# Kernel optimization log

Measured on AMD Instinct MI355X. Metric: run time of the kernel, lower is better.

Reference implementation:

```python
import jax, jax.numpy as jnp
import numpy as np

E, K = 8, 2            # num_experts, top_k
H, DFF = 1024, 2048    # embd_dim, d_ff
B, S = 4, 1024


def setup_inputs() -> dict:
    key = jax.random.key(0)
    ks = jax.random.split(key, 5)
    s_in = 1.0 / np.sqrt(H)
    s_ff = 1.0 / np.sqrt(DFF)
    return {
        "x": jax.random.normal(ks[0], (B, S, H), jnp.float32),
        "centroids": jax.random.normal(ks[1], (E, H), jnp.float32),
        # nn.Linear weights are [out, in]
        "gate_w": jax.random.normal(ks[2], (E, DFF, H), jnp.float32) * s_in,
        "up_w": jax.random.normal(ks[3], (E, DFF, H), jnp.float32) * s_in,
        "down_w": jax.random.normal(ks[4], (E, H, DFF), jnp.float32) * s_ff,
        "routing_bias": jnp.zeros((E,), jnp.float32),
    }


def reference(x, centroids, gate_w, up_w, down_w, routing_bias):
    Bb, Ss, Hh = x.shape
    xf = x.reshape(-1, Hh)  # [T, H]
    # sigmoid affinity router + (non-trainable) routing bias
    affinity = jax.nn.sigmoid(xf @ centroids.T)          # [T, E]
    topk_scores, topk_idx = jax.lax.top_k(affinity + routing_bias, K)  # [T, K]
    topk_w = jax.nn.softmax(topk_scores, axis=-1)        # [T, K]

    # Dense per-expert SwiGLU FFN on all tokens (same math as the
    # sort/gather grouped loop; selection happens in the gather below).
    g = jnp.einsum('th,efh->etf', xf, gate_w)            # [E, T, DFF]
    u = jnp.einsum('th,efh->etf', xf, up_w)              # [E, T, DFF]
    y = jnp.einsum('etf,ehf->eth', jax.nn.silu(g) * u, down_w)  # [E, T, H]

    yt = jnp.transpose(y, (1, 0, 2))                     # [T, E, H]
    sel = jnp.take_along_axis(yt, topk_idx[:, :, None], axis=1)  # [T, K, H]
    out_flat = jnp.sum(sel * topk_w[:, :, None], axis=1)  # [T, H]

    counts = jnp.bincount(topk_idx.ravel(), length=E)    # per-expert token counts
    return out_flat.reshape(Bb, Ss, Hh), counts
```

## Files before the change

### kernel.cpp

```cpp
#include <hip/hip_runtime.h>
#include <math.h>

constexpr int E = 8, H = 1024, DFF = 2048, T = 4096;
constexpr int TR = 8192;
constexpr int BK = 32;

typedef __bf16 bf16x8 __attribute__((ext_vector_type(8)));
typedef __bf16 bf16x4 __attribute__((ext_vector_type(4)));
typedef float f32x4 __attribute__((ext_vector_type(4)));

__device__ __forceinline__ void gload16(const void* g, void* l) {
    __builtin_amdgcn_global_load_lds(
        (const __attribute__((address_space(1))) unsigned int*)g,
        (__attribute__((address_space(3))) unsigned int*)l, 16, 0, 0);
}

__global__ __launch_bounds__(256) void k1_affinity(
    const float* __restrict__ x, const float* __restrict__ cent,
    const float* __restrict__ bias,
    int* __restrict__ se, float* __restrict__ sw) {
    __shared__ float cs[E * H];
    int tid = threadIdx.x;
    for (int i = tid; i < E * H / 4; i += 256)
        ((float4*)cs)[i] = ((const float4*)cent)[i];
    __syncthreads();

    int wave = tid >> 6, lane = tid & 63;
    int t = blockIdx.x * 4 + wave;
    const float4* xr = (const float4*)(x + (size_t)t * H);
    float acc[E] = {};
    #pragma unroll
    for (int it = 0; it < 4; it++) {
        float4 xv = xr[lane + it * 64];
        #pragma unroll
        for (int e = 0; e < E; e++) {
            float4 cv = ((const float4*)(cs + e * H))[lane + it * 64];
            acc[e] = fmaf(xv.x, cv.x, acc[e]);
            acc[e] = fmaf(xv.y, cv.y, acc[e]);
            acc[e] = fmaf(xv.z, cv.z, acc[e]);
            acc[e] = fmaf(xv.w, cv.w, acc[e]);
        }
    }
    #pragma unroll
    for (int off = 32; off; off >>= 1)
        #pragma unroll
        for (int e = 0; e < E; e++) acc[e] += __shfl_down(acc[e], off);

    if (lane == 0) {
        float s[E];
        #pragma unroll
        for (int e = 0; e < E; e++)
            s[e] = 1.0f / (1.0f + expf(-acc[e])) + bias[e];
        int i0 = 0;
        for (int e = 1; e < E; e++) if (s[e] > s[i0]) i0 = e;
        int i1 = -1;
        for (int e = 0; e < E; e++) {
            if (e == i0) continue;
            if (i1 < 0 || s[e] > s[i1]) i1 = e;
        }
        float m = fmaxf(s[i0], s[i1]);
        float w0 = expf(s[i0] - m), w1 = expf(s[i1] - m);
        float inv = 1.0f / (w0 + w1);
        se[2 * t] = i0;     sw[2 * t] = w0 * inv;
        se[2 * t + 1] = i1; sw[2 * t + 1] = w1 * inv;
    }
}

__global__ __launch_bounds__(256) void k1b_partition(
    const int* __restrict__ se, int* __restrict__ token_list,
    int* __restrict__ sp, int* __restrict__ cnt) {
    int e = blockIdx.x;
    int tid = threadIdx.x;
    int wave = tid >> 6, lane = tid & 63;
    __shared__ int wsum[4];
    int running = 0;
    for (int c0 = 0; c0 < 2 * T; c0 += 256) {
        int i = c0 + tid;
        bool pred = (se[i] == e);
        unsigned long long mask = __ballot(pred);
        int pos_in_wave = __popcll(mask & ((1ull << lane) - 1ull));
        if (lane == 0) wsum[wave] = __popcll(mask);
        __syncthreads();
        int wbase = 0;
        for (int w2 = 0; w2 < wave; w2++) wbase += wsum[w2];
        int total = wsum[0] + wsum[1] + wsum[2] + wsum[3];
        if (pred) {
            int p = running + wbase + pos_in_wave;
            token_list[e * T + p] = i >> 1;
            sp[i] = p;
        }
        running += total;
        __syncthreads();
    }
    if (tid == 0) cnt[e] = running;
}

__global__ void k15_offsets(const int* __restrict__ cnt, int* __restrict__ off,
                            float* __restrict__ out_counts) {
    if (threadIdx.x == 0) {
        int acc = 0;
        for (int e = 0; e < E; e++) { off[e] = acc; acc += cnt[e]; }
    }
    if (threadIdx.x < E) out_counts[threadIdx.x] = (float)cnt[threadIdx.x];
}

__global__ __launch_bounds__(256) void k_conv(const float* __restrict__ in,
                                              __bf16* __restrict__ out, int n4) {
    int i = blockIdx.x * 256 + threadIdx.x;
    if (i < n4) {
        float4 v = ((const float4*)in)[i];
        bf16x4 o = {(__bf16)v.x, (__bf16)v.y, (__bf16)v.z, (__bf16)v.w};
        ((bf16x4*)out)[i] = o;
    }
}

__global__ __launch_bounds__(256) void k2_gateup(
    const __bf16* __restrict__ xb, const __bf16* __restrict__ gwb,
    const __bf16* __restrict__ uwb, const int* __restrict__ cnt,
    const int* __restrict__ off, const int* __restrict__ token_list,
    __bf16* __restrict__ h) {
    int bid = blockIdx.x;
    int e = bid >> 10;
    int rem = bid & 1023;
    int mt = rem >> 5;
    int nt = rem & 31;
    int Me = cnt[e];
    if (mt * 128 >= Me) return;
    int offe = off[e];

    __shared__ __bf16 As[128 * 32];
    __shared__ __bf16 Bg[64 * 32];
    __shared__ __bf16 Bu[64 * 32];

    int tid = threadIdx.x;
    int lane = tid & 63, w = tid >> 6;
    int wm = w >> 1, wn = w & 1;

    int l0 = tid, l1 = 256 + tid;
    int ar0 = l0 >> 2, akq0 = (l0 & 3) ^ ((ar0 >> 1) & 3);
    int ar1 = l1 >> 2, akq1 = (l1 & 3) ^ ((ar1 >> 1) & 3);
    int row0 = mt * 128 + ar0; if (row0 >= Me) row0 = Me - 1;
    int row1 = mt * 128 + ar1; if (row1 >= Me) row1 = Me - 1;
    int tok0 = token_list[e * T + row0];
    int tok1 = token_list[e * T + row1];
    const __bf16* asrc0 = xb + (size_t)tok0 * H + akq0 * 8;
    const __bf16* asrc1 = xb + (size_t)tok1 * H + akq1 * 8;
    const __bf16* gsrc = gwb + ((size_t)e * DFF + nt * 64 + ar0) * H + akq0 * 8;
    const __bf16* usrc = uwb + ((size_t)e * DFF + nt * 64 + ar0) * H + akq0 * 8;

    f32x4 accg[4][2] = {};
    f32x4 accu[4][2] = {};

    int kq = lane >> 4;
    int m15 = lane & 15;

    for (int k0 = 0; k0 < H; k0 += BK) {
        gload16(asrc0 + k0, &As[l0 * 8]);
        gload16(asrc1 + k0, &As[l1 * 8]);
        gload16(gsrc + k0, &Bg[tid * 8]);
        gload16(usrc + k0, &Bu[tid * 8]);
        __syncthreads();

        bf16x8 af[4], gf[2], uf[2];
        #pragma unroll
        for (int i = 0; i < 4; i++) {
            int row = wm * 64 + i * 16 + m15;
            int slot = kq ^ ((row >> 1) & 3);
            af[i] = *(const bf16x8*)&As[row * 32 + slot * 8];
        }
        #pragma unroll
        for (int j = 0; j < 2; j++) {
            int row = wn * 32 + j * 16 + m15;
            int slot = kq ^ ((row >> 1) & 3);
            gf[j] = *(const bf16x8*)&Bg[row * 32 + slot * 8];
            uf[j] = *(const bf16x8*)&Bu[row * 32 + slot * 8];
        }
        #pragma unroll
        for (int i = 0; i < 4; i++)
            #pragma unroll
            for (int j = 0; j < 2; j++) {
                accg[i][j] = __builtin_amdgcn_mfma_f32_16x16x32_bf16(af[i], gf[j], accg[i][j], 0, 0, 0);
                accu[i][j] = __builtin_amdgcn_mfma_f32_16x16x32_bf16(af[i], uf[j], accu[i][j], 0, 0, 0);
            }
        __syncthreads();
    }

    #pragma unroll
    for (int i = 0; i < 4; i++)
        #pragma unroll
        for (int j = 0; j < 2; j++) {
            int nloc = wn * 32 + j * 16 + m15;
            size_t c = (size_t)nt * 64 + nloc;
            #pragma unroll
            for (int p = 0; p < 4; p++) {
                int mloc = wm * 64 + i * 16 + kq * 4 + p;
                int mrow = mt * 128 + mloc;
                if (mrow < Me) {
                    float g = accg[i][j][p], u = accu[i][j][p];
                    float sig = 1.0f / (1.0f + __expf(-g));
                    h[(size_t)(offe + mrow) * DFF + c] = (__bf16)(g * sig * u);
                }
            }
        }
}

__global__ __launch_bounds__(256) void k3_down(
    const __bf16* __restrict__ h, const __bf16* __restrict__ dwb,
    const int* __restrict__ cnt, const int* __restrict__ off,
    __bf16* __restrict__ y) {
    int bid = blockIdx.x;
    int e = bid >> 8;
    int rem = bid & 255;
    int mt = rem >> 3;
    int nt = rem & 7;
    int Me = cnt[e];
    if (mt * 128 >= Me) return;
    int offe = off[e];

    __shared__ __bf16 As[128 * 32];
    __shared__ __bf16 Bs[128 * 32];

    int tid = threadIdx.x;
    int lane = tid & 63, w = tid >> 6;
    int wm = w >> 1, wn = w & 1;

    int l0 = tid, l1 = 256 + tid;
    int r0 = l0 >> 2, kq0 = (l0 & 3) ^ ((r0 >> 1) & 3);
    int r1 = l1 >> 2, kq1 = (l1 & 3) ^ ((r1 >> 1) & 3);
    int arow_g0 = offe + mt * 128 + r0; if (arow_g0 > TR - 1) arow_g0 = TR - 1;
    int arow_g1 = offe + mt * 128 + r1; if (arow_g1 > TR - 1) arow_g1 = TR - 1;
    const __bf16* asrc0 = h + (size_t)arow_g0 * DFF + kq0 * 8;
    const __bf16* asrc1 = h + (size_t)arow_g1 * DFF + kq1 * 8;
    const __bf16* bsrc0 = dwb + ((size_t)e * H + nt * 128 + r0) * DFF + kq0 * 8;
    const __bf16* bsrc1 = dwb + ((size_t)e * H + nt * 128 + r1) * DFF + kq1 * 8;

    f32x4 acc[4][4] = {};
    int kq = lane >> 4;
    int m15 = lane & 15;

    for (int k0 = 0; k0 < DFF; k0 += BK) {
        gload16(asrc0 + k0, &As[l0 * 8]);
        gload16(asrc1 + k0, &As[l1 * 8]);
        gload16(bsrc0 + k0, &Bs[l0 * 8]);
        gload16(bsrc1 + k0, &Bs[l1 * 8]);
        __syncthreads();

        bf16x8 af[4], bf[4];
        #pragma unroll
        for (int i = 0; i < 4; i++) {
            int row = wm * 64 + i * 16 + m15;
            int slot = kq ^ ((row >> 1) & 3);
            af[i] = *(const bf16x8*)&As[row * 32 + slot * 8];
        }
        #pragma unroll
        for (int j = 0; j < 4; j++) {
            int row = wn * 64 + j * 16 + m15;
            int slot = kq ^ ((row >> 1) & 3);
            bf[j] = *(const bf16x8*)&Bs[row * 32 + slot * 8];
        }
        #pragma unroll
        for (int i = 0; i < 4; i++)
            #pragma unroll
            for (int j = 0; j < 4; j++)
                acc[i][j] = __builtin_amdgcn_mfma_f32_16x16x32_bf16(af[i], bf[j], acc[i][j], 0, 0, 0);
        __syncthreads();
    }

    #pragma unroll
    for (int i = 0; i < 4; i++)
        #pragma unroll
        for (int j = 0; j < 4; j++) {
            int nglob = nt * 128 + wn * 64 + j * 16 + m15;
            #pragma unroll
            for (int p = 0; p < 4; p++) {
                int mloc = wm * 64 + i * 16 + kq * 4 + p;
                int mrow = mt * 128 + mloc;
                if (mrow < Me)
                    y[(size_t)(offe + mrow) * H + nglob] = (__bf16)acc[i][j][p];
            }
        }
}

__global__ __launch_bounds__(256) void k_gather(
    const __bf16* __restrict__ y, const int* __restrict__ se,
    const int* __restrict__ sp, const float* __restrict__ sw,
    const int* __restrict__ off, float* __restrict__ out) {
    int t = blockIdx.x;
    int r0 = off[se[2 * t]] + sp[2 * t];
    int r1 = off[se[2 * t + 1]] + sp[2 * t + 1];
    float w0 = sw[2 * t], w1 = sw[2 * t + 1];
    const bf16x4* y0 = (const bf16x4*)(y + (size_t)r0 * H);
    const bf16x4* y1 = (const bf16x4*)(y + (size_t)r1 * H);
    float4* o = (float4*)(out + (size_t)t * H);
    int c = threadIdx.x;
    bf16x4 a = y0[c], b = y1[c];
    float4 v;
    v.x = w0 * (float)a[0] + w1 * (float)b[0];
    v.y = w0 * (float)a[1] + w1 * (float)b[1];
    v.z = w0 * (float)a[2] + w1 * (float)b[2];
    v.w = w0 * (float)a[3] + w1 * (float)b[3];
    o[c] = v;
}

extern "C" void kernel_launch(void* const* d_in, const int* in_sizes, int n_in,
                              void* d_out, int out_size, void* d_ws, size_t ws_size,
                              hipStream_t stream) {
    const float* x    = (const float*)d_in[0];
    const float* cent = (const float*)d_in[1];
    const float* gw   = (const float*)d_in[2];
    const float* uw   = (const float*)d_in[3];
    const float* dw   = (const float*)d_in[4];
    const float* bias = (const float*)d_in[5];
    float* out = (float*)d_out;

    char* ws = (char*)d_ws;
    int*   cnt        = (int*)(ws + 0);
    int*   off        = (int*)(ws + 64);
    int*   se         = (int*)(ws + 128);
    int*   sp         = (int*)(ws + 128 + 32768);
    float* sw         = (float*)(ws + 128 + 65536);
    int*   token_list = (int*)(ws + 128 + 98304);
    const size_t MB = 1u << 20;
    __bf16* gwb = (__bf16*)(ws + 1 * MB);
    __bf16* uwb = (__bf16*)(ws + 1 * MB + 33554432);
    __bf16* dwb = gwb;
    __bf16* y   = uwb;
    __bf16* xb  = (__bf16*)(ws + 1 * MB + 67108864);
    __bf16* h   = (__bf16*)(ws + 1 * MB + 75497472);

    const int W4 = E * DFF * H / 4;
    const int X4 = T * H / 4;

    k_conv<<<(W4 + 255) / 256, 256, 0, stream>>>(gw, gwb, W4);
    k_conv<<<(W4 + 255) / 256, 256, 0, stream>>>(uw, uwb, W4);
    k_conv<<<(X4 + 255) / 256, 256, 0, stream>>>(x, xb, X4);
    k1_affinity<<<T / 4, 256, 0, stream>>>(x, cent, bias, se, sw);
    k1b_partition<<<E, 256, 0, stream>>>(se, token_list, sp, cnt);
    k15_offsets<<<1, 64, 0, stream>>>(cnt, off, out + (size_t)T * H);
    k2_gateup<<<E * 32 * 32, 256, 0, stream>>>(xb, gwb, uwb, cnt, off, token_list, h);
    k_conv<<<(W4 + 255) / 256, 256, 0, stream>>>(dw, dwb, W4);
    k3_down<<<E * 32 * 8, 256, 0, stream>>>(h, dwb, cnt, off, y);
    k_gather<<<T, 256, 0, stream>>>(y, se, sp, sw, off, out);
}
```

Measured before the change: 440.4 us.

## Compact MoE GEMM job list, double K-tile depth, and fuse conversion kernels

Builds a compact list of active (expert, M-tile) jobs in the offsets kernel so the grouped GEMMs launch only about as many blocks as there are real tiles, instead of launching the full expert by M-tile grid and exiting early. Both GEMM kernels now stage K-tiles of 64 rather than 32 with an 8-way XOR swizzle, halving the number of barriers and loop iterations per output tile. The three fp32-to-bf16 conversions for the gate and up weights and for x are merged into one launch. LDS use per block doubles, which may reduce occupancy.

```diff
diff --git a/kernel.cpp b/kernel.cpp
--- a/kernel.cpp
+++ b/kernel.cpp
@@ -3,7 +3,7 @@
 
 constexpr int E = 8, H = 1024, DFF = 2048, T = 4096;
 constexpr int TR = 8192;
-constexpr int BK = 32;
+constexpr int MAXJ = 72;
 
 typedef __bf16 bf16x8 __attribute__((ext_vector_type(8)));
 typedef __bf16 bf16x4 __attribute__((ext_vector_type(4)));
@@ -96,10 +96,16 @@
 }
 
 __global__ void k15_offsets(const int* __restrict__ cnt, int* __restrict__ off,
-                            float* __restrict__ out_counts) {
+                            float* __restrict__ out_counts,
+                            int* __restrict__ jobs, int* __restrict__ njobs) {
     if (threadIdx.x == 0) {
-        int acc = 0;
-        for (int e = 0; e < E; e++) { off[e] = acc; acc += cnt[e]; }
+        int acc = 0, nj = 0;
+        for (int e = 0; e < E; e++) {
+            off[e] = acc; acc += cnt[e];
+            int mts = (cnt[e] + 127) >> 7;
+            for (int mt = 0; mt < mts; mt++) jobs[nj++] = e * 64 + mt;
+        }
+        njobs[0] = nj;
     }
     if (threadIdx.x < E) out_counts[threadIdx.x] = (float)cnt[threadIdx.x];
 }
@@ -114,74 +120,99 @@
     }
 }
 
+__global__ __launch_bounds__(256) void k_conv3(
+    const float* __restrict__ gw, __bf16* __restrict__ gwb,
+    const float* __restrict__ uw, __bf16* __restrict__ uwb,
+    const float* __restrict__ x, __bf16* __restrict__ xb,
+    int w4, int x4) {
+    int i = blockIdx.x * 256 + threadIdx.x;
+    const float* in; __bf16* out; int idx;
+    if (i < w4) { in = gw; out = gwb; idx = i; }
+    else if (i < 2 * w4) { in = uw; out = uwb; idx = i - w4; }
+    else { idx = i - 2 * w4; if (idx >= x4) return; in = x; out = xb; }
+    float4 v = ((const float4*)in)[idx];
+    bf16x4 o = {(__bf16)v.x, (__bf16)v.y, (__bf16)v.z, (__bf16)v.w};
+    ((bf16x4*)out)[idx] = o;
+}
+
 __global__ __launch_bounds__(256) void k2_gateup(
     const __bf16* __restrict__ xb, const __bf16* __restrict__ gwb,
     const __bf16* __restrict__ uwb, const int* __restrict__ cnt,
     const int* __restrict__ off, const int* __restrict__ token_list,
+    const int* __restrict__ jobs, const int* __restrict__ njobs,
     __bf16* __restrict__ h) {
-    int bid = blockIdx.x;
-    int e = bid >> 10;
-    int rem = bid & 1023;
-    int mt = rem >> 5;
-    int nt = rem & 31;
-    int Me = cnt[e];
-    if (mt * 128 >= Me) return;
-    int offe = off[e];
-
-    __shared__ __bf16 As[128 * 32];
-    __shared__ __bf16 Bg[64 * 32];
-    __shared__ __bf16 Bu[64 * 32];
+    int jt = blockIdx.x >> 5, nt = blockIdx.x & 31;
+    if (jt >= njobs[0]) return;
+    int job = jobs[jt];
+    int e = job >> 6, mt = job & 63;
+    int Me = cnt[e], offe = off[e];
+
+    __shared__ __bf16 As[128 * 64];
+    __shared__ __bf16 Bg[64 * 64];
+    __shared__ __bf16 Bu[64 * 64];
 
     int tid = threadIdx.x;
     int lane = tid & 63, w = tid >> 6;
     int wm = w >> 1, wn = w & 1;
 
-    int l0 = tid, l1 = 256 + tid;
-    int ar0 = l0 >> 2, akq0 = (l0 & 3) ^ ((ar0 >> 1) & 3);
-    int ar1 = l1 >> 2, akq1 = (l1 & 3) ^ ((ar1 >> 1) & 3);
-    int row0 = mt * 128 + ar0; if (row0 >= Me) row0 = Me - 1;
-    int row1 = mt * 128 + ar1; if (row1 >= Me) row1 = Me - 1;
-    int tok0 = token_list[e * T + row0];
-    int tok1 = token_list[e * T + row1];
-    const __bf16* asrc0 = xb + (size_t)tok0 * H + akq0 * 8;
-    const __bf16* asrc1 = xb + (size_t)tok1 * H + akq1 * 8;
-    const __bf16* gsrc = gwb + ((size_t)e * DFF + nt * 64 + ar0) * H + akq0 * 8;
-    const __bf16* usrc = uwb + ((size_t)e * DFF + nt * 64 + ar0) * H + akq0 * 8;
+    const __bf16* asrc[4];
+    #pragma unroll
+    for (int rr = 0; rr < 4; rr++) {
+        int l = rr * 256 + tid;
+        int row = l >> 3, sl = l & 7;
+        int gr = mt * 128 + row; if (gr >= Me) gr = Me - 1;
+        int tok = token_list[e * T + gr];
+        asrc[rr] = xb + (size_t)tok * H + ((sl ^ (row & 7)) * 8);
+    }
+    const __bf16 *bsg[2], *bsu[2];
+    #pragma unroll
+    for (int rr = 0; rr < 2; rr++) {
+        int l = rr * 256 + tid;
+        int row = l >> 3, sl = l & 7;
+        size_t base = ((size_t)e * DFF + nt * 64 + row) * H + ((sl ^ (row & 7)) * 8);
+        bsg[rr] = gwb + base;
+        bsu[rr] = uwb + base;
+    }
 
     f32x4 accg[4][2] = {};
     f32x4 accu[4][2] = {};
-
-    int kq = lane >> 4;
-    int m15 = lane & 15;
-
-    for (int k0 = 0; k0 < H; k0 += BK) {
-        gload16(asrc0 + k0, &As[l0 * 8]);
-        gload16(asrc1 + k0, &As[l1 * 8]);
-        gload16(gsrc + k0, &Bg[tid * 8]);
-        gload16(usrc + k0, &Bu[tid * 8]);
-        __syncthreads();
-
-        bf16x8 af[4], gf[2], uf[2];
-        #pragma unroll
-        for (int i = 0; i < 4; i++) {
-            int row = wm * 64 + i * 16 + m15;
-            int slot = kq ^ ((row >> 1) & 3);
-            af[i] = *(const bf16x8*)&As[row * 32 + slot * 8];
-        }
-        #pragma unroll
-        for (int j = 0; j < 2; j++) {
-            int row = wn * 32 + j * 16 + m15;
-            int slot = kq ^ ((row >> 1) & 3);
-            gf[j] = *(const bf16x8*)&Bg[row * 32 + slot * 8];
-            uf[j] = *(const bf16x8*)&Bu[row * 32 + slot * 8];
-        }
-        #pragma unroll
-        for (int i = 0; i < 4; i++)
+    int kq = lane >> 4, m15 = lane & 15;
+
+    for (int k0 = 0; k0 < H; k0 += 64) {
+        #pragma unroll
+        for (int rr = 0; rr < 4; rr++)
+            gload16(asrc[rr] + k0, &As[(rr * 256 + tid) * 8]);
+        #pragma unroll
+        for (int rr = 0; rr < 2; rr++) {
+            gload16(bsg[rr] + k0, &Bg[(rr * 256 + tid) * 8]);
+            gload16(bsu[rr] + k0, &Bu[(rr * 256 + tid) * 8]);
+        }
+        __syncthreads();
+
+        #pragma unroll
+        for (int kc = 0; kc < 2; kc++) {
+            bf16x8 af[4], gf[2], uf[2];
+            #pragma unroll
+            for (int i = 0; i < 4; i++) {
+                int row = wm * 64 + i * 16 + m15;
+                int sl = (kc * 4 + kq) ^ (row & 7);
+                af[i] = *(const bf16x8*)&As[row * 64 + sl * 8];
+            }
             #pragma unroll
             for (int j = 0; j < 2; j++) {
-                accg[i][j] = __builtin_amdgcn_mfma_f32_16x16x32_bf16(af[i], gf[j], accg[i][j], 0, 0, 0);
-                accu[i][j] = __builtin_amdgcn_mfma_f32_16x16x32_bf16(af[i], uf[j], accu[i][j], 0, 0, 0);
-            }
+                int row = wn * 32 + j * 16 + m15;
+                int sl = (kc * 4 + kq) ^ (row & 7);
+                gf[j] = *(const bf16x8*)&Bg[row * 64 + sl * 8];
+                uf[j] = *(const bf16x8*)&Bu[row * 64 + sl * 8];
+            }
+            #pragma unroll
+            for (int i = 0; i < 4; i++)
+                #pragma unroll
+                for (int j = 0; j < 2; j++) {
+                    accg[i][j] = __builtin_amdgcn_mfma_f32_16x16x32_bf16(af[i], gf[j], accg[i][j], 0, 0, 0);
+                    accu[i][j] = __builtin_amdgcn_mfma_f32_16x16x32_bf16(af[i], uf[j], accu[i][j], 0, 0, 0);
+                }
+        }
         __syncthreads();
     }
 
@@ -207,62 +238,64 @@
 __global__ __launch_bounds__(256) void k3_down(
     const __bf16* __restrict__ h, const __bf16* __restrict__ dwb,
     const int* __restrict__ cnt, const int* __restrict__ off,
+    const int* __restrict__ jobs, const int* __restrict__ njobs,
     __bf16* __restrict__ y) {
-    int bid = blockIdx.x;
-    int e = bid >> 8;
-    int rem = bid & 255;
-    int mt = rem >> 3;
-    int nt = rem & 7;
-    int Me = cnt[e];
-    if (mt * 128 >= Me) return;
-    int offe = off[e];
-
-    __shared__ __bf16 As[128 * 32];
-    __shared__ __bf16 Bs[128 * 32];
+    int jt = blockIdx.x >> 3, nt = blockIdx.x & 7;
+    if (jt >= njobs[0]) return;
+    int job = jobs[jt];
+    int e = job >> 6, mt = job & 63;
+    int Me = cnt[e], offe = off[e];
+
+    __shared__ __bf16 As[128 * 64];
+    __shared__ __bf16 Bs[128 * 64];
 
     int tid = threadIdx.x;
     int lane = tid & 63, w = tid >> 6;
     int wm = w >> 1, wn = w & 1;
 
-    int l0 = tid, l1 = 256 + tid;
-    int r0 = l0 >> 2, kq0 = (l0 & 3) ^ ((r0 >> 1) & 3);
-    int r1 = l1 >> 2, kq1 = (l1 & 3) ^ ((r1 >> 1) & 3);
-    int arow_g0 = offe + mt * 128 + r0; if (arow_g0 > TR - 1) arow_g0 = TR - 1;
-    int arow_g1 = offe + mt * 128 + r1; if (arow_g1 > TR - 1) arow_g1 = TR - 1;
-    const __bf16* asrc0 = h + (size_t)arow_g0 * DFF + kq0 * 8;
-    const __bf16* asrc1 = h + (size_t)arow_g1 * DFF + kq1 * 8;
-    const __bf16* bsrc0 = dwb + ((size_t)e * H + nt * 128 + r0) * DFF + kq0 * 8;
-    const __bf16* bsrc1 = dwb + ((size_t)e * H + nt * 128 + r1) * DFF + kq1 * 8;
+    const __bf16 *asrc[4], *bsrc[4];
+    #pragma unroll
+    for (int rr = 0; rr < 4; rr++) {
+        int l = rr * 256 + tid;
+        int row = l >> 3, sl = l & 7;
+        int koff = (sl ^ (row & 7)) * 8;
+        int gr = mt * 128 + row; if (gr >= Me) gr = Me - 1;
+        asrc[rr] = h + (size_t)(offe + gr) * DFF + koff;
+        bsrc[rr] = dwb + ((size_t)e * H + nt * 128 + row) * DFF + koff;
+    }
 
     f32x4 acc[4][4] = {};
-    int kq = lane >> 4;
-    int m15 = lane & 15;
-
-    for (int k0 = 0; k0 < DFF; k0 += BK) {
-        gload16(asrc0 + k0, &As[l0 * 8]);
-        gload16(asrc1 + k0, &As[l1 * 8]);
-        gload16(bsrc0 + k0, &Bs[l0 * 8]);
-        gload16(bsrc1 + k0, &Bs[l1 * 8]);
-        __syncthreads();
-
-        bf16x8 af[4], bf[4];
-        #pragma unroll
-        for (int i = 0; i < 4; i++) {
-            int row = wm * 64 + i * 16 + m15;
-            int slot = kq ^ ((row >> 1) & 3);
-            af[i] = *(const bf16x8*)&As[row * 32 + slot * 8];
-        }
-        #pragma unroll
-        for (int j = 0; j < 4; j++) {
-            int row = wn * 64 + j * 16 + m15;
-            int slot = kq ^ ((row >> 1) & 3);
-            bf[j] = *(const bf16x8*)&Bs[row * 32 + slot * 8];
-        }
-        #pragma unroll
-        for (int i = 0; i < 4; i++)
-            #pragma unroll
-            for (int j = 0; j < 4; j++)
-                acc[i][j] = __builtin_amdgcn_mfma_f32_16x16x32_bf16(af[i], bf[j], acc[i][j], 0, 0, 0);
+    int kq = lane >> 4, m15 = lane & 15;
+
+    for (int k0 = 0; k0 < DFF; k0 += 64) {
+        #pragma unroll
+        for (int rr = 0; rr < 4; rr++) {
+            gload16(asrc[rr] + k0, &As[(rr * 256 + tid) * 8]);
+            gload16(bsrc[rr] + k0, &Bs[(rr * 256 + tid) * 8]);
+        }
+        __syncthreads();
+
+        #pragma unroll
+        for (int kc = 0; kc < 2; kc++) {
+            bf16x8 af[4], bf[4];
+            #pragma unroll
+            for (int i = 0; i < 4; i++) {
+                int row = wm * 64 + i * 16 + m15;
+                int sl = (kc * 4 + kq) ^ (row & 7);
+                af[i] = *(const bf16x8*)&As[row * 64 + sl * 8];
+            }
+            #pragma unroll
+            for (int j = 0; j < 4; j++) {
+                int row = wn * 64 + j * 16 + m15;
+                int sl = (kc * 4 + kq) ^ (row & 7);
+                bf[j] = *(const bf16x8*)&Bs[row * 64 + sl * 8];
+            }
+            #pragma unroll
+            for (int i = 0; i < 4; i++)
+                #pragma unroll
+                for (int j = 0; j < 4; j++)
+                    acc[i][j] = __builtin_amdgcn_mfma_f32_16x16x32_bf16(af[i], bf[j], acc[i][j], 0, 0, 0);
+        }
         __syncthreads();
     }
 
@@ -320,6 +353,8 @@
     int*   sp         = (int*)(ws + 128 + 32768);
     float* sw         = (float*)(ws + 128 + 65536);
     int*   token_list = (int*)(ws + 128 + 98304);
+    int*   jobs       = (int*)(ws + 229504);
+    int*   njobs      = (int*)(ws + 229824);
     const size_t MB = 1u << 20;
     __bf16* gwb = (__bf16*)(ws + 1 * MB);
     __bf16* uwb = (__bf16*)(ws + 1 * MB + 33554432);
@@ -330,15 +365,14 @@
 
     const int W4 = E * DFF * H / 4;
     const int X4 = T * H / 4;
-
-    k_conv<<<(W4 + 255) / 256, 256, 0, stream>>>(gw, gwb, W4);
-    k_conv<<<(W4 + 255) / 256, 256, 0, stream>>>(uw, uwb, W4);
-    k_conv<<<(X4 + 255) / 256, 256, 0, stream>>>(x, xb, X4);
+    const int C3 = 2 * W4 + X4;
+
+    k_conv3<<<(C3 + 255) / 256, 256, 0, stream>>>(gw, gwb, uw, uwb, x, xb, W4, X4);
     k1_affinity<<<T / 4, 256, 0, stream>>>(x, cent, bias, se, sw);
     k1b_partition<<<E, 256, 0, stream>>>(se, token_list, sp, cnt);
-    k15_offsets<<<1, 64, 0, stream>>>(cnt, off, out + (size_t)T * H);
-    k2_gateup<<<E * 32 * 32, 256, 0, stream>>>(xb, gwb, uwb, cnt, off, token_list, h);
+    k15_offsets<<<1, 64, 0, stream>>>(cnt, off, out + (size_t)T * H, jobs, njobs);
+    k2_gateup<<<MAXJ * 32, 256, 0, stream>>>(xb, gwb, uwb, cnt, off, token_list, jobs, njobs, h);
     k_conv<<<(W4 + 255) / 256, 256, 0, stream>>>(dw, dwb, W4);
-    k3_down<<<E * 32 * 8, 256, 0, stream>>>(h, dwb, cnt, off, y);
+    k3_down<<<MAXJ * 8, 256, 0, stream>>>(h, dwb, cnt, off, jobs, njobs, y);
     k_gather<<<T, 256, 0, stream>>>(y, se, sp, sw, off, out);
 }
```

Result: faster. 418.0 us (-5.1%).
